# Kernel tuning notes

Hardware: AMD Instinct MI355X
Metric: run time of the kernel (lower is better)

Reference implementation:

```python
import jax, jax.numpy as jnp
import numpy as np

N_X, N_Y, D = 8192, 512, None  # D set below
D = 512

def setup_inputs() -> dict:
    key = jax.random.key(0)
    kx, ky = jax.random.split(key)
    x = jax.random.normal(kx, (8192, D), dtype=jnp.float32)
    y = jax.random.normal(ky, (8192, D), dtype=jnp.float32)
    gamma = jnp.float32(1.0)  # learnable scalar parameter, init value from __init__
    return {"x": x, "y": y, "gamma": gamma}

def reference(x, y, gamma):
    # K_{ij} = exp(-gamma * ||x_i - y_j||^2)
    x2 = jnp.sum(x * x, axis=1)[:, None]          # [n_x, 1]
    y2 = jnp.sum(y * y, axis=1)[None, :]          # [1, n_y]
    xy = x @ y.T                                  # [n_x, n_y] GEMM
    sq = jnp.maximum(x2 + y2 - 2.0 * xy, 0.0)     # clamp tiny negatives from cancellation
    return jnp.exp(-gamma * sq)
```

## Files before the change

kernel.cpp:

```cpp
#include <hip/hip_runtime.h>
#include <hip/hip_bf16.h>

typedef unsigned char u8;
typedef unsigned short u16;
typedef unsigned int u32;
typedef int i32x8 __attribute__((ext_vector_type(8)));
typedef float f32x4 __attribute__((ext_vector_type(4)));

#define NX 8192
#define NY 8192
#define D  512
#define BM 128
#define BN 128
#define BK 128

#define SCALE_ONE 0x7F7F7F7F

__device__ __forceinline__ void async16(void* lds, const void* g) {
    __builtin_amdgcn_global_load_lds(
        (const __attribute__((address_space(1))) void*)g,
        (__attribute__((address_space(3))) void*)lds,
        16, 0, 0);
}

__global__ __launch_bounds__(256) void prep_kernel(
    const float* __restrict__ x, const float* __restrict__ y,
    u8* __restrict__ xq, u8* __restrict__ yq,
    float* __restrict__ x2, float* __restrict__ y2)
{
    const int lane = threadIdx.x & 63;
    const int row  = blockIdx.x * 4 + (threadIdx.x >> 6);
    const float* src; u8* dst; float* nrm;
    if (row < NX) {
        src = x + (size_t)row * D; dst = xq + (size_t)row * D; nrm = x2 + row;
    } else {
        const int r = row - NX;
        src = y + (size_t)r * D; dst = yq + (size_t)r * D; nrm = y2 + r;
    }
    float4 v0 = *(const float4*)(src + lane * 8);
    float4 v1 = *(const float4*)(src + lane * 8 + 4);
    float s = v0.x*v0.x + v0.y*v0.y + v0.z*v0.z + v0.w*v0.w
            + v1.x*v1.x + v1.y*v1.y + v1.z*v1.z + v1.w*v1.w;
    u32 p0 = 0, p1 = 0;
    p0 = __builtin_amdgcn_cvt_pk_fp8_f32(v0.x, v0.y, p0, false);
    p0 = __builtin_amdgcn_cvt_pk_fp8_f32(v0.z, v0.w, p0, true);
    p1 = __builtin_amdgcn_cvt_pk_fp8_f32(v1.x, v1.y, p1, false);
    p1 = __builtin_amdgcn_cvt_pk_fp8_f32(v1.z, v1.w, p1, true);
    uint2 pk = make_uint2(p0, p1);
    *(uint2*)(dst + lane * 8) = pk;

    #pragma unroll
    for (int o = 32; o > 0; o >>= 1) s += __shfl_down(s, o);
    if (lane == 0) *nrm = s;
}

__global__ __launch_bounds__(256) void rbf_kernel(
    const u8* __restrict__ xq, const u8* __restrict__ yq,
    const float* __restrict__ x2, const float* __restrict__ y2,
    const float* __restrict__ gamma_p, float* __restrict__ out)
{
    __shared__ u8 As[2][BM * BK];
    __shared__ u8 Bs[2][BN * BK];

    const int t    = threadIdx.x;
    const int lane = t & 63;
    const int wid  = t >> 6;
    const int wr   = wid >> 1;
    const int wc   = wid & 1;

    const int nwg = gridDim.x;
    const int cpx = nwg >> 3;
    const int bid = blockIdx.x;
    const int swz = (bid & 7) * cpx + (bid >> 3);
    const int brow = swz >> 6;
    const int bcol = swz & 63;

    const size_t row0 = (size_t)brow * BM;
    const size_t col0 = (size_t)bcol * BN;

    const int c0 = wid * 4;
    const int lr = lane >> 3;
    const int lc = (lane & 7) * 16;

    auto stage = [&](int buf, int kt) {
        #pragma unroll
        for (int i = 0; i < 4; ++i) {
            const int c = c0 + i;
            async16(&As[buf][c * 1024], xq + (row0 + (size_t)(c * 8 + lr)) * D + kt + lc);
        }
        #pragma unroll
        for (int i = 0; i < 4; ++i) {
            const int c = c0 + i;
            async16(&Bs[buf][c * 1024], yq + (col0 + (size_t)(c * 8 + lr)) * D + kt + lc);
        }
    };

    stage(0, 0);
    __syncthreads();

    f32x4 acc[4][4] = {};
    const int ko = (lane >> 4) * 32;
    const int ar = (lane & 15);

    #pragma unroll
    for (int kt = 0; kt < 4; ++kt) {
        if (kt < 3) stage((kt + 1) & 1, (kt + 1) * BK);
        const int cur = kt & 1;
        i32x8 a[4], b[4];
        #pragma unroll
        for (int m = 0; m < 4; ++m)
            a[m] = *(const i32x8*)&As[cur][(wr * 64 + m * 16 + ar) * BK + ko];
        #pragma unroll
        for (int n = 0; n < 4; ++n)
            b[n] = *(const i32x8*)&Bs[cur][(wc * 64 + n * 16 + ar) * BK + ko];
        #pragma unroll
        for (int m = 0; m < 4; ++m)
            #pragma unroll
            for (int n = 0; n < 4; ++n)
                acc[m][n] = __builtin_amdgcn_mfma_scale_f32_16x16x128_f8f6f4(
                    a[m], b[n], acc[m][n],
                    0 , 0 ,
                    0, SCALE_ONE, 0, SCALE_ONE);
        if (kt < 3) __syncthreads();
    }

    const float gamma = *gamma_p;
    const int rl = (lane >> 4) * 4;
    const int cl = lane & 15;
    #pragma unroll
    for (int m = 0; m < 4; ++m) {
        #pragma unroll
        for (int j = 0; j < 4; ++j) {
            const size_t gr = row0 + wr * 64 + m * 16 + rl + j;
            const float xn = x2[gr];
            float* orow = out + gr * (size_t)NY + col0 + wc * 64 + cl;
            #pragma unroll
            for (int n = 0; n < 4; ++n) {
                const float yn = y2[col0 + wc * 64 + n * 16 + cl];
                float sq = xn + yn - 2.0f * acc[m][n][j];
                sq = fmaxf(sq, 0.0f);
                orow[n * 16] = __expf(-gamma * sq);
            }
        }
    }
}

extern "C" void kernel_launch(void* const* d_in, const int* in_sizes, int n_in,
                              void* d_out, int out_size, void* d_ws, size_t ws_size,
                              hipStream_t stream) {
    const float* x = (const float*)d_in[0];
    const float* y = (const float*)d_in[1];
    const float* gamma_p = (const float*)d_in[2];
    float* out = (float*)d_out;

    u8* xq = (u8*)d_ws;
    u8* yq = xq + (size_t)NX * D;
    float* x2 = (float*)(yq + (size_t)NY * D);
    float* y2 = x2 + NX;

    prep_kernel<<<(NX + NY) / 4, 256, 0, stream>>>(x, y, xq, yq, x2, y2);

    const int grid = (NX / BM) * (NY / BN);
    rbf_kernel<<<grid, 256, 0, stream>>>(xq, yq, x2, y2, gamma_p, out);
}
```

Measured before the change: 320.8 us.

## Make blocks persistent over column tiles with the A panel resident in LDS

Each block now loads its full 128xD fp8 X panel into LDS once and loops over 16 column tiles, streaming Y chunks through a double buffer with a continuous prefetch that crosses tile boundaries. The grid shrinks from 4096 blocks to 256, which removes repeated X loads and per-block launch and prologue overhead. In exchange, LDS use rises to 96KB per block, which limits occupancy. The epilogue stores are also serialized with the next tile's compute inside each block instead of being overlapped across many independent blocks.

```diff
diff --git a/kernel.cpp b/kernel.cpp
--- a/kernel.cpp
+++ b/kernel.cpp
@@ -13,6 +13,8 @@
 #define BM 128
 #define BN 128
 #define BK 128
+#define NKT 4
+#define TPB 16
 
 #define SCALE_ONE 0x7F7F7F7F
 
@@ -59,8 +61,8 @@
     const float* __restrict__ x2, const float* __restrict__ y2,
     const float* __restrict__ gamma_p, float* __restrict__ out)
 {
-    __shared__ u8 As[2][BM * BK];
-    __shared__ u8 Bs[2][BN * BK];
+    __shared__ u8 Al[NKT * BM * BK];
+    __shared__ u8 Bl[2][BN * BK];
 
     const int t    = threadIdx.x;
     const int lane = t & 63;
@@ -68,78 +70,91 @@
     const int wr   = wid >> 1;
     const int wc   = wid & 1;
 
-    const int nwg = gridDim.x;
-    const int cpx = nwg >> 3;
-    const int bid = blockIdx.x;
-    const int swz = (bid & 7) * cpx + (bid >> 3);
-    const int brow = swz >> 6;
-    const int bcol = swz & 63;
+    const int bid  = blockIdx.x;
+    const int brow = bid >> 2;
+    const int bg   = bid & 3;
 
     const size_t row0 = (size_t)brow * BM;
-    const size_t col0 = (size_t)bcol * BN;
 
-    const int c0 = wid * 4;
     const int lr = lane >> 3;
     const int lc = (lane & 7) * 16;
 
-    auto stage = [&](int buf, int kt) {
+    #pragma unroll
+    for (int i = 0; i < 16; ++i) {
+        const int c  = wid * 16 + i;
+        const int kt = c >> 4;
+        const int cc = c & 15;
+        async16(&Al[c * 1024],
+                xq + (row0 + (size_t)(cc * 8 + lr)) * D + kt * BK + lc);
+    }
+    {
+        const size_t col0 = (size_t)(bg * 16 + 0) * BN;
         #pragma unroll
         for (int i = 0; i < 4; ++i) {
-            const int c = c0 + i;
-            async16(&As[buf][c * 1024], xq + (row0 + (size_t)(c * 8 + lr)) * D + kt + lc);
+            const int c = wid * 4 + i;
+            async16(&Bl[0][c * 1024],
+                    yq + (col0 + (size_t)(c * 8 + lr)) * D + 0 * BK + lc);
         }
-        #pragma unroll
-        for (int i = 0; i < 4; ++i) {
-            const int c = c0 + i;
-            async16(&Bs[buf][c * 1024], yq + (col0 + (size_t)(c * 8 + lr)) * D + kt + lc);
-        }
-    };
-
-    stage(0, 0);
+    }
     __syncthreads();
 
-    f32x4 acc[4][4] = {};
+    const float gamma = *gamma_p;
     const int ko = (lane >> 4) * 32;
     const int ar = (lane & 15);
+    const int rl = (lane >> 4) * 4;
+    const int cl = lane & 15;
 
-    #pragma unroll
-    for (int kt = 0; kt < 4; ++kt) {
-        if (kt < 3) stage((kt + 1) & 1, (kt + 1) * BK);
-        const int cur = kt & 1;
-        i32x8 a[4], b[4];
+    int cur = 0;
+    for (int tt = 0; tt < TPB; ++tt) {
+        f32x4 acc[4][4] = {};
         #pragma unroll
-        for (int m = 0; m < 4; ++m)
-            a[m] = *(const i32x8*)&As[cur][(wr * 64 + m * 16 + ar) * BK + ko];
-        #pragma unroll
-        for (int n = 0; n < 4; ++n)
-            b[n] = *(const i32x8*)&Bs[cur][(wc * 64 + n * 16 + ar) * BK + ko];
-        #pragma unroll
-        for (int m = 0; m < 4; ++m)
+        for (int kt = 0; kt < NKT; ++kt) {
+            const int nchunk = tt * NKT + kt + 1;
+            if (nchunk < TPB * NKT) {
+                const int ntt = nchunk >> 2;
+                const int nkt = nchunk & 3;
+                const size_t ncol0 = (size_t)(bg * 16 + ntt) * BN;
+                #pragma unroll
+                for (int i = 0; i < 4; ++i) {
+                    const int c = wid * 4 + i;
+                    async16(&Bl[cur ^ 1][c * 1024],
+                            yq + (ncol0 + (size_t)(c * 8 + lr)) * D + nkt * BK + lc);
+                }
+            }
+            i32x8 a[4], b[4];
+            #pragma unroll
+            for (int m = 0; m < 4; ++m)
+                a[m] = *(const i32x8*)&Al[kt * (BM * BK) + (wr * 64 + m * 16 + ar) * BK + ko];
             #pragma unroll
             for (int n = 0; n < 4; ++n)
-                acc[m][n] = __builtin_amdgcn_mfma_scale_f32_16x16x128_f8f6f4(
-                    a[m], b[n], acc[m][n],
-                    0 , 0 ,
-                    0, SCALE_ONE, 0, SCALE_ONE);
-        if (kt < 3) __syncthreads();
-    }
+                b[n] = *(const i32x8*)&Bl[cur][(wc * 64 + n * 16 + ar) * BK + ko];
+            #pragma unroll
+            for (int m = 0; m < 4; ++m)
+                #pragma unroll
+                for (int n = 0; n < 4; ++n)
+                    acc[m][n] = __builtin_amdgcn_mfma_scale_f32_16x16x128_f8f6f4(
+                        a[m], b[n], acc[m][n],
+                        0 , 0 ,
+                        0, SCALE_ONE, 0, SCALE_ONE);
+            __syncthreads();
+            cur ^= 1;
+        }
 
-    const float gamma = *gamma_p;
-    const int rl = (lane >> 4) * 4;
-    const int cl = lane & 15;
-    #pragma unroll
-    for (int m = 0; m < 4; ++m) {
+        const size_t col0 = (size_t)(bg * 16 + tt) * BN;
         #pragma unroll
-        for (int j = 0; j < 4; ++j) {
-            const size_t gr = row0 + wr * 64 + m * 16 + rl + j;
-            const float xn = x2[gr];
-            float* orow = out + gr * (size_t)NY + col0 + wc * 64 + cl;
+        for (int m = 0; m < 4; ++m) {
             #pragma unroll
-            for (int n = 0; n < 4; ++n) {
-                const float yn = y2[col0 + wc * 64 + n * 16 + cl];
-                float sq = xn + yn - 2.0f * acc[m][n][j];
-                sq = fmaxf(sq, 0.0f);
-                orow[n * 16] = __expf(-gamma * sq);
+            for (int j = 0; j < 4; ++j) {
+                const size_t gr = row0 + wr * 64 + m * 16 + rl + j;
+                const float xn = x2[gr];
+                float* orow = out + gr * (size_t)NY + col0 + wc * 64 + cl;
+                #pragma unroll
+                for (int n = 0; n < 4; ++n) {
+                    const float yn = y2[col0 + wc * 64 + n * 16 + cl];
+                    float sq = xn + yn - 2.0f * acc[m][n][j];
+                    sq = fmaxf(sq, 0.0f);
+                    orow[n * 16] = __expf(-gamma * sq);
+                }
             }
         }
     }
@@ -160,6 +175,5 @@
 
     prep_kernel<<<(NX + NY) / 4, 256, 0, stream>>>(x, y, xq, yq, x2, y2);
 
-    const int grid = (NX / BM) * (NY / BN);
-    rbf_kernel<<<grid, 256, 0, stream>>>(xq, yq, x2, y2, gamma_p, out);
+    rbf_kernel<<<256, 256, 0, stream>>>(xq, yq, x2, y2, gamma_p, out);
 }
```

New measurement: 366.1 us. +14.1%, slower.

## Load FP8 GEMM operands directly from global memory, dropping LDS staging

Applied to the files above, without the earlier changes.

Removes the double-buffered LDS staging with async global-to-LDS loads and barriers. Each wave now reads its MFMA operand fragments straight from global memory into registers, and launch bounds request two blocks per SM. The aim is to remove LDS traffic and synchronisation and to raise occupancy, since K is only 512 and the kernel is likely bound by output stores. The cost is duplicated global and L2 reads across waves, plus less latency hiding within a block.

```diff
diff --git a/kernel.cpp b/kernel.cpp
--- a/kernel.cpp
+++ b/kernel.cpp
@@ -2,7 +2,6 @@
 #include <hip/hip_bf16.h>
 
 typedef unsigned char u8;
-typedef unsigned short u16;
 typedef unsigned int u32;
 typedef int i32x8 __attribute__((ext_vector_type(8)));
 typedef float f32x4 __attribute__((ext_vector_type(4)));
@@ -15,13 +14,6 @@
 #define BK 128
 
 #define SCALE_ONE 0x7F7F7F7F
-
-__device__ __forceinline__ void async16(void* lds, const void* g) {
-    __builtin_amdgcn_global_load_lds(
-        (const __attribute__((address_space(1))) void*)g,
-        (__attribute__((address_space(3))) void*)lds,
-        16, 0, 0);
-}
 
 __global__ __launch_bounds__(256) void prep_kernel(
     const float* __restrict__ x, const float* __restrict__ y,
@@ -54,14 +46,11 @@
     if (lane == 0) *nrm = s;
 }
 
-__global__ __launch_bounds__(256) void rbf_kernel(
+__global__ __launch_bounds__(256, 2) void rbf_kernel(
     const u8* __restrict__ xq, const u8* __restrict__ yq,
     const float* __restrict__ x2, const float* __restrict__ y2,
     const float* __restrict__ gamma_p, float* __restrict__ out)
 {
-    __shared__ u8 As[2][BM * BK];
-    __shared__ u8 Bs[2][BN * BK];
-
     const int t    = threadIdx.x;
     const int lane = t & 63;
     const int wid  = t >> 6;
@@ -78,41 +67,29 @@
     const size_t row0 = (size_t)brow * BM;
     const size_t col0 = (size_t)bcol * BN;
 
-    const int c0 = wid * 4;
-    const int lr = lane >> 3;
-    const int lc = (lane & 7) * 16;
-
-    auto stage = [&](int buf, int kt) {
-        #pragma unroll
-        for (int i = 0; i < 4; ++i) {
-            const int c = c0 + i;
-            async16(&As[buf][c * 1024], xq + (row0 + (size_t)(c * 8 + lr)) * D + kt + lc);
-        }
-        #pragma unroll
-        for (int i = 0; i < 4; ++i) {
-            const int c = c0 + i;
-            async16(&Bs[buf][c * 1024], yq + (col0 + (size_t)(c * 8 + lr)) * D + kt + lc);
-        }
-    };
-
-    stage(0, 0);
-    __syncthreads();
-
-    f32x4 acc[4][4] = {};
     const int ko = (lane >> 4) * 32;
     const int ar = (lane & 15);
 
+    const u8* ap[4];
+    const u8* bp[4];
+    #pragma unroll
+    for (int m = 0; m < 4; ++m)
+        ap[m] = xq + (row0 + (size_t)(wr * 64 + m * 16 + ar)) * D + ko;
+    #pragma unroll
+    for (int n = 0; n < 4; ++n)
+        bp[n] = yq + (col0 + (size_t)(wc * 64 + n * 16 + ar)) * D + ko;
+
+    f32x4 acc[4][4] = {};
+
     #pragma unroll
     for (int kt = 0; kt < 4; ++kt) {
-        if (kt < 3) stage((kt + 1) & 1, (kt + 1) * BK);
-        const int cur = kt & 1;
         i32x8 a[4], b[4];
         #pragma unroll
         for (int m = 0; m < 4; ++m)
-            a[m] = *(const i32x8*)&As[cur][(wr * 64 + m * 16 + ar) * BK + ko];
+            a[m] = *(const i32x8*)(ap[m] + kt * BK);
         #pragma unroll
         for (int n = 0; n < 4; ++n)
-            b[n] = *(const i32x8*)&Bs[cur][(wc * 64 + n * 16 + ar) * BK + ko];
+            b[n] = *(const i32x8*)(bp[n] + kt * BK);
         #pragma unroll
         for (int m = 0; m < 4; ++m)
             #pragma unroll
@@ -121,7 +98,6 @@
                     a[m], b[n], acc[m][n],
                     0 , 0 ,
                     0, SCALE_ONE, 0, SCALE_ONE);
-        if (kt < 3) __syncthreads();
     }
 
     const float gamma = *gamma_p;
```

Result: slower. 390.2 us (+21.6%).
